# Optimization experiments

Measured on AMD Instinct MI355X. Metric: run time of the kernel, lower is better.

## Reference

```python
import jax, jax.numpy as jnp
import numpy as np

B, N, C, H = 8, 1024, 1024, 16
HD = C // H
SCALE = HD ** -0.5

def setup_inputs() -> dict:
    key = jax.random.key(0)
    k1, k2, k3, k4 = jax.random.split(key, 4)
    x = jax.random.normal(k1, (B, N, C), dtype=jnp.float32)
    # torch nn.Linear weights: [out, in]
    w_qkv = jax.random.normal(k2, (3 * C, C), dtype=jnp.float32) * (C ** -0.5)
    w_proj = jax.random.normal(k3, (C, C), dtype=jnp.float32) * (C ** -0.5)
    b_proj = jax.random.normal(k4, (C,), dtype=jnp.float32) * 0.02
    return {"x": x, "w_qkv": w_qkv, "w_proj": w_proj, "b_proj": b_proj}

def reference(x, w_qkv, w_proj, b_proj):
    Bv, Nv, Cv = x.shape
    # qkv projection (no bias); torch Linear: x @ W^T
    qkv = jnp.einsum('bnc,dc->bnd', x, w_qkv)
    qkv = qkv.reshape(Bv, Nv, 3, H, HD).transpose(2, 0, 3, 1, 4)  # [3,B,H,N,hd]
    q, k, v = qkv[0], qkv[1], qkv[2]
    attn = jnp.einsum('bhnd,bhmd->bhnm', q, k) * SCALE  # [B,H,N,N]
    attn = jax.nn.softmax(attn, axis=-1)
    out = jnp.einsum('bhnm,bhmd->bhnd', attn, v)
    out = out.transpose(0, 2, 1, 3).reshape(Bv, Nv, Cv)
    out = jnp.einsum('bnc,dc->bnd', out, w_proj) + b_proj
    return out
```

## Files before the change

kernel.cpp:

```cpp
#include <hip/hip_runtime.h>


typedef __attribute__((ext_vector_type(8))) short bf16x8;
typedef __attribute__((ext_vector_type(4))) short bf16x4;
typedef __attribute__((ext_vector_type(4))) float f32x4;

__device__ __forceinline__ short f2bf(float f) {
    union { float f; unsigned u; } x;
    x.f = f;
    unsigned r = x.u + 0x7fffu + ((x.u >> 16) & 1u);
    return (short)(r >> 16);
}

__device__ __forceinline__ void load_lds16(const void* g, void* l) {
    __builtin_amdgcn_global_load_lds((const __attribute__((address_space(1))) unsigned*)g,
                                     (__attribute__((address_space(3))) unsigned*)l,
                                     16, 0, 0);
}

__global__ __launch_bounds__(256) void convert_all(const float* __restrict__ x,
                                                   const float* __restrict__ wqkv,
                                                   const float* __restrict__ wproj,
                                                   short* __restrict__ xb,
                                                   short* __restrict__ wqkvb,
                                                   short* __restrict__ wprojb) {
    int i = blockIdx.x * 256 + threadIdx.x;
    const float* src;
    short* dst;
    int j;
    if (i < 2097152)      { src = x;     dst = xb;     j = i; }
    else if (i < 2883584) { src = wqkv;  dst = wqkvb;  j = i - 2097152; }
    else                  { src = wproj; dst = wprojb; j = i - 2883584; }
    float4 v = *(const float4*)(src + j * 4);
    unsigned lo = (unsigned short)f2bf(v.x) | ((unsigned)(unsigned short)f2bf(v.y) << 16);
    unsigned hi = (unsigned short)f2bf(v.z) | ((unsigned)(unsigned short)f2bf(v.w) << 16);
    uint2 p; p.x = lo; p.y = hi;
    *(uint2*)(dst + j * 4) = p;
}

__global__ __launch_bounds__(256, 4) void gemm_qkv(const short* __restrict__ A,
                                                   const short* __restrict__ Bt,
                                                   short* __restrict__ q,
                                                   short* __restrict__ k,
                                                   short* __restrict__ vt) {
    __shared__ alignas(16) short As[2][128][32];
    __shared__ alignas(16) short Bs[2][128][32];
    const int K = 1024;
    const int m0 = blockIdx.y * 128;
    const int n0 = blockIdx.x * 128;
    const int t = threadIdx.x;
    const int w = t >> 6, lane = t & 63, quad = lane >> 4, l16 = lane & 15;
    const int wm = (w >> 1) * 64, wn = (w & 1) * 64;
    const int srow = lane >> 2;
    const int sc8 = (((lane & 3) ^ ((lane >> 3) & 3))) * 8;
    const int cq  = (quad ^ ((l16 >> 1) & 3)) * 8;

    const short* Abase = &A[(m0 + w * 32 + srow) * K + sc8];
    const short* Bbase = &Bt[(n0 + w * 32 + srow) * K + sc8];

    f32x4 acc[4][4];
    for (int mi = 0; mi < 4; ++mi)
        for (int ni = 0; ni < 4; ++ni)
            acc[mi][ni] = (f32x4){0.f, 0.f, 0.f, 0.f};

    load_lds16(Abase,          &As[0][w * 32][0]);
    load_lds16(Abase + 16 * K, &As[0][w * 32 + 16][0]);
    load_lds16(Bbase,          &Bs[0][w * 32][0]);
    load_lds16(Bbase + 16 * K, &Bs[0][w * 32 + 16][0]);

    #pragma unroll
    for (int it = 0; it < 32; ++it) {
        const int cur = it & 1;
        asm volatile("s_waitcnt vmcnt(0) lgkmcnt(0)" ::: "memory");
        asm volatile("s_barrier" ::: "memory");
        if (it < 31) {
            const int nb = cur ^ 1;
            load_lds16(Abase + (it + 1) * 32,          &As[nb][w * 32][0]);
            load_lds16(Abase + 16 * K + (it + 1) * 32, &As[nb][w * 32 + 16][0]);
            load_lds16(Bbase + (it + 1) * 32,          &Bs[nb][w * 32][0]);
            load_lds16(Bbase + 16 * K + (it + 1) * 32, &Bs[nb][w * 32 + 16][0]);
        }
        bf16x8 af[4], bfr[4];
        for (int i = 0; i < 4; ++i) af[i]  = *(const bf16x8*)&As[cur][wm + i * 16 + l16][cq];
        for (int i = 0; i < 4; ++i) bfr[i] = *(const bf16x8*)&Bs[cur][wn + i * 16 + l16][cq];
        for (int mi = 0; mi < 4; ++mi)
            for (int ni = 0; ni < 4; ++ni)
                acc[mi][ni] = __builtin_amdgcn_mfma_f32_16x16x32_bf16(af[mi], bfr[ni], acc[mi][ni], 0, 0, 0);
    }

    const float QS = 0.125f * 1.44269504088896f;
    for (int ni = 0; ni < 4; ++ni) {
        int col = n0 + wn + ni * 16 + l16;
        int sect = col >> 10;
        int c = col & 1023;
        int h = c >> 6, d = c & 63;
        for (int mi = 0; mi < 4; ++mi) {
            for (int r = 0; r < 4; ++r) {
                int m = m0 + wm + mi * 16 + quad * 4 + r;
                int b = m >> 10, i = m & 1023;
                float v = acc[mi][ni][r];
                if (sect == 0)      q[((b * 16 + h) * 1024 + i) * 64 + d] = f2bf(v * QS);
                else if (sect == 1) k[((b * 16 + h) * 1024 + i) * 64 + d] = f2bf(v);
                else                vt[((b * 16 + h) * 64 + d) * 1024 + i] = f2bf(v);
            }
        }
    }
}

__global__ __launch_bounds__(256) void attn_kernel(const short* __restrict__ q,
                                                   const short* __restrict__ k,
                                                   const short* __restrict__ vt,
                                                   short* __restrict__ ao) {
    __shared__ alignas(16) short Ks[2][64][72];
    __shared__ alignas(16) short Vs[2][64][72];

    const int bh = blockIdx.y, qt = blockIdx.x;
    const int t = threadIdx.x, w = t >> 6, lane = t & 63, quad = lane >> 4, l16 = lane & 15;
    const short* qg = q  + (bh * 1024 + qt * 128) * 64;
    const short* kg = k  + bh * 65536;
    const short* vg = vt + bh * 65536;

    bf16x8 qf[2][2];
    for (int mi = 0; mi < 2; ++mi) {
        const short* qr = qg + (w * 32 + mi * 16 + l16) * 64;
        qf[mi][0] = *(const bf16x8*)(qr + quad * 8);
        qf[mi][1] = *(const bf16x8*)(qr + 32 + quad * 8);
    }

    const int r0 = t >> 3,          c80 = (t & 7) * 8;
    const int r1 = (t + 256) >> 3,  c81 = c80;

    float rs[2] = {0.f, 0.f};
    f32x4 oaccT[2][4];
    for (int mi = 0; mi < 2; ++mi)
        for (int dt = 0; dt < 4; ++dt) oaccT[mi][dt] = (f32x4){0.f, 0.f, 0.f, 0.f};

    {
        float4 a = *(const float4*)&kg[r0 * 64 + c80];
        float4 b = *(const float4*)&kg[r1 * 64 + c81];
        float4 c = *(const float4*)&vg[r0 * 1024 + c80];
        float4 d = *(const float4*)&vg[r1 * 1024 + c81];
        *(float4*)&Ks[0][r0][c80] = a;  *(float4*)&Ks[0][r1][c81] = b;
        *(float4*)&Vs[0][r0][c80] = c;  *(float4*)&Vs[0][r1][c81] = d;
    }

    for (int jt = 0; jt < 16; ++jt) {
        const int cur = jt & 1;
        asm volatile("s_waitcnt lgkmcnt(0)" ::: "memory");
        asm volatile("s_barrier" ::: "memory");

        float4 kr0, kr1, vr0, vr1;
        if (jt < 15) {
            int jn = jt + 1;
            kr0 = *(const float4*)&kg[(jn * 64 + r0) * 64 + c80];
            kr1 = *(const float4*)&kg[(jn * 64 + r1) * 64 + c81];
            vr0 = *(const float4*)&vg[r0 * 1024 + jn * 64 + c80];
            vr1 = *(const float4*)&vg[r1 * 1024 + jn * 64 + c81];
        }

        for (int js = 0; js < 4; ++js) {
            bf16x8 kf0 = *(const bf16x8*)&Ks[cur][js * 16 + l16][quad * 8];
            bf16x8 kf1 = *(const bf16x8*)&Ks[cur][js * 16 + l16][32 + quad * 8];
            bf16x4 vtf[4];
            for (int dt = 0; dt < 4; ++dt)
                vtf[dt] = *(const bf16x4*)&Vs[cur][dt * 16 + l16][js * 16 + quad * 4];
            for (int mi = 0; mi < 2; ++mi) {
                f32x4 s = (f32x4){0.f, 0.f, 0.f, 0.f};
                s = __builtin_amdgcn_mfma_f32_16x16x32_bf16(kf0, qf[mi][0], s, 0, 0, 0);
                s = __builtin_amdgcn_mfma_f32_16x16x32_bf16(kf1, qf[mi][1], s, 0, 0, 0);
                bf16x4 pfrag;
                for (int r = 0; r < 4; ++r) {
                    float p = __builtin_amdgcn_exp2f(s[r]);
                    rs[mi] += p;
                    pfrag[r] = f2bf(p);
                }
                for (int dt = 0; dt < 4; ++dt)
                    oaccT[mi][dt] = __builtin_amdgcn_mfma_f32_16x16x16bf16_1k(
                        vtf[dt], pfrag, oaccT[mi][dt], 0, 0, 0);
            }
        }

        if (jt < 15) {
            const int nxt = cur ^ 1;
            *(float4*)&Ks[nxt][r0][c80] = kr0;  *(float4*)&Ks[nxt][r1][c81] = kr1;
            *(float4*)&Vs[nxt][r0][c80] = vr0;  *(float4*)&Vs[nxt][r1][c81] = vr1;
        }
    }

    for (int mi = 0; mi < 2; ++mi) {
        rs[mi] += __shfl_xor(rs[mi], 16, 64);
        rs[mi] += __shfl_xor(rs[mi], 32, 64);
    }

    const int b = bh >> 4, h = bh & 15;
    for (int mi = 0; mi < 2; ++mi) {
        float inv = 1.0f / rs[mi];
        int i = qt * 128 + w * 32 + mi * 16 + l16;
        short* aor = ao + (b * 1024 + i) * 1024 + h * 64;
        for (int dt = 0; dt < 4; ++dt) {
            bf16x4 o4;
            for (int r = 0; r < 4; ++r) o4[r] = f2bf(oaccT[mi][dt][r] * inv);
            *(bf16x4*)(aor + dt * 16 + quad * 4) = o4;
        }
    }
}

__global__ __launch_bounds__(256, 4) void gemm_proj(const short* __restrict__ A,
                                                    const short* __restrict__ Bt,
                                                    const float* __restrict__ bias,
                                                    float* __restrict__ out) {
    __shared__ alignas(16) short As[2][128][32];
    __shared__ alignas(16) short Bs[2][128][32];
    const int K = 1024;
    const int m0 = blockIdx.y * 128;
    const int n0 = blockIdx.x * 128;
    const int t = threadIdx.x;
    const int w = t >> 6, lane = t & 63, quad = lane >> 4, l16 = lane & 15;
    const int wm = (w >> 1) * 64, wn = (w & 1) * 64;
    const int srow = lane >> 2;
    const int sc8 = (((lane & 3) ^ ((lane >> 3) & 3))) * 8;
    const int cq  = (quad ^ ((l16 >> 1) & 3)) * 8;

    const short* Abase = &A[(m0 + w * 32 + srow) * K + sc8];
    const short* Bbase = &Bt[(n0 + w * 32 + srow) * K + sc8];

    f32x4 acc[4][4];
    for (int mi = 0; mi < 4; ++mi)
        for (int ni = 0; ni < 4; ++ni)
            acc[mi][ni] = (f32x4){0.f, 0.f, 0.f, 0.f};

    load_lds16(Abase,          &As[0][w * 32][0]);
    load_lds16(Abase + 16 * K, &As[0][w * 32 + 16][0]);
    load_lds16(Bbase,          &Bs[0][w * 32][0]);
    load_lds16(Bbase + 16 * K, &Bs[0][w * 32 + 16][0]);

    #pragma unroll
    for (int it = 0; it < 32; ++it) {
        const int cur = it & 1;
        asm volatile("s_waitcnt vmcnt(0) lgkmcnt(0)" ::: "memory");
        asm volatile("s_barrier" ::: "memory");
        if (it < 31) {
            const int nb = cur ^ 1;
            load_lds16(Abase + (it + 1) * 32,          &As[nb][w * 32][0]);
            load_lds16(Abase + 16 * K + (it + 1) * 32, &As[nb][w * 32 + 16][0]);
            load_lds16(Bbase + (it + 1) * 32,          &Bs[nb][w * 32][0]);
            load_lds16(Bbase + 16 * K + (it + 1) * 32, &Bs[nb][w * 32 + 16][0]);
        }
        bf16x8 af[4], bfr[4];
        for (int i = 0; i < 4; ++i) af[i]  = *(const bf16x8*)&As[cur][wm + i * 16 + l16][cq];
        for (int i = 0; i < 4; ++i) bfr[i] = *(const bf16x8*)&Bs[cur][wn + i * 16 + l16][cq];
        for (int mi = 0; mi < 4; ++mi)
            for (int ni = 0; ni < 4; ++ni)
                acc[mi][ni] = __builtin_amdgcn_mfma_f32_16x16x32_bf16(af[mi], bfr[ni], acc[mi][ni], 0, 0, 0);
    }

    for (int ni = 0; ni < 4; ++ni) {
        int col = n0 + wn + ni * 16 + l16;
        float bv = bias[col];
        for (int mi = 0; mi < 4; ++mi) {
            for (int r = 0; r < 4; ++r) {
                int m = m0 + wm + mi * 16 + quad * 4 + r;
                out[m * 1024 + col] = acc[mi][ni][r] + bv;
            }
        }
    }
}

extern "C" void kernel_launch(void* const* d_in, const int* in_sizes, int n_in,
                              void* d_out, int out_size, void* d_ws, size_t ws_size,
                              hipStream_t stream) {
    const float* x      = (const float*)d_in[0];
    const float* w_qkv  = (const float*)d_in[1];
    const float* w_proj = (const float*)d_in[2];
    const float* b_proj = (const float*)d_in[3];
    float* out = (float*)d_out;

    char* ws = (char*)d_ws;
    short* xb     = (short*)(ws);
    short* wqkvb  = (short*)(ws + 16777216);
    short* wprojb = (short*)(ws + 23068672);
    short* qb     = (short*)(ws + 25165824);
    short* kb     = (short*)(ws + 41943040);
    short* vtb    = (short*)(ws + 58720256);
    short* aob    = (short*)(ws + 75497472);

    convert_all<<<12288, 256, 0, stream>>>(x, w_qkv, w_proj, xb, wqkvb, wprojb);
    gemm_qkv<<<dim3(24, 64), 256, 0, stream>>>(xb, wqkvb, qb, kb, vtb);
    attn_kernel<<<dim3(8, 128), 256, 0, stream>>>(qb, kb, vtb, aob);
    gemm_proj<<<dim3(8, 64), 256, 0, stream>>>(aob, wprojb, b_proj, out);
}
```

Baseline: 268.4 us.

## Replace both GEMMs with a 256x256 tile, 8-wave, deeply pipelined kernel

Both linear projections now use one templated GEMM with 256x256 output tiles, 512 threads, BK=64 and a double-buffered 128KB dynamic LDS layout with XOR swizzling. Global-to-LDS loads are spread across four MFMA phases with partial vmcnt waits, and s_setprio raises priority around the MFMA blocks. The aim is to raise arithmetic intensity and overlap loads with MFMA work. Block indices are remapped so neighbouring blocks share row panels in cache. The cost is fewer blocks, only 128 for the projection GEMM on 256 CUs, along with higher register and LDS pressure.

Result: no change. 266.9 us (-0.6%).

```diff
diff --git a/kernel.cpp b/kernel.cpp
--- a/kernel.cpp
+++ b/kernel.cpp
@@ -38,70 +38,175 @@
     *(uint2*)(dst + j * 4) = p;
 }
 
-__global__ __launch_bounds__(256, 4) void gemm_qkv(const short* __restrict__ A,
-                                                   const short* __restrict__ Bt,
-                                                   short* __restrict__ q,
-                                                   short* __restrict__ k,
-                                                   short* __restrict__ vt) {
-    __shared__ alignas(16) short As[2][128][32];
-    __shared__ alignas(16) short Bs[2][128][32];
+template<int EPI, int NTX>
+__global__ __launch_bounds__(512, 2) void gemm256(const short* __restrict__ A,
+                                                  const short* __restrict__ Bt,
+                                                  short* __restrict__ q,
+                                                  short* __restrict__ kk,
+                                                  short* __restrict__ vt,
+                                                  const float* __restrict__ bias,
+                                                  float* __restrict__ out) {
+    extern __shared__ short lds[];
+    short* const As = lds;
+    short* const Bs = lds + 32768;
     const int K = 1024;
-    const int m0 = blockIdx.y * 128;
-    const int n0 = blockIdx.x * 128;
+
+    constexpr int CHUNK = NTX * 4;
+    const int bid = blockIdx.x;
+    const int tile = (bid & 7) * CHUNK + (bid >> 3);
+    const int m0 = (tile / NTX) * 256;
+    const int n0 = (tile % NTX) * 256;
+
     const int t = threadIdx.x;
     const int w = t >> 6, lane = t & 63, quad = lane >> 4, l16 = lane & 15;
-    const int wm = (w >> 1) * 64, wn = (w & 1) * 64;
-    const int srow = lane >> 2;
-    const int sc8 = (((lane & 3) ^ ((lane >> 3) & 3))) * 8;
-    const int cq  = (quad ^ ((l16 >> 1) & 3)) * 8;
-
-    const short* Abase = &A[(m0 + w * 32 + srow) * K + sc8];
-    const short* Bbase = &Bt[(n0 + w * 32 + srow) * K + sc8];
-
-    f32x4 acc[4][4];
-    for (int mi = 0; mi < 4; ++mi)
-        for (int ni = 0; ni < 4; ++ni)
-            acc[mi][ni] = (f32x4){0.f, 0.f, 0.f, 0.f};
-
-    load_lds16(Abase,          &As[0][w * 32][0]);
-    load_lds16(Abase + 16 * K, &As[0][w * 32 + 16][0]);
-    load_lds16(Bbase,          &Bs[0][w * 32][0]);
-    load_lds16(Bbase + 16 * K, &Bs[0][w * 32 + 16][0]);
-
+    const int wm = (w >> 2) * 128, wn = (w & 3) * 64;
+    const int sw = l16 & 7;
+
+    const int srow = t >> 3;
+    const int scol = ((t & 7) ^ (srow & 7)) * 8;
+    const short* Ag = A  + (m0 + srow) * K + scol;
+    const short* Bg = Bt + (n0 + srow) * K + scol;
+    short* const Asw = As + (w * 8) * 64;
+    short* const Bsw = Bs + (w * 8) * 64;
+
+    f32x4 acc[8][4];
     #pragma unroll
-    for (int it = 0; it < 32; ++it) {
-        const int cur = it & 1;
-        asm volatile("s_waitcnt vmcnt(0) lgkmcnt(0)" ::: "memory");
-        asm volatile("s_barrier" ::: "memory");
-        if (it < 31) {
-            const int nb = cur ^ 1;
-            load_lds16(Abase + (it + 1) * 32,          &As[nb][w * 32][0]);
-            load_lds16(Abase + 16 * K + (it + 1) * 32, &As[nb][w * 32 + 16][0]);
-            load_lds16(Bbase + (it + 1) * 32,          &Bs[nb][w * 32][0]);
-            load_lds16(Bbase + 16 * K + (it + 1) * 32, &Bs[nb][w * 32 + 16][0]);
-        }
-        bf16x8 af[4], bfr[4];
-        for (int i = 0; i < 4; ++i) af[i]  = *(const bf16x8*)&As[cur][wm + i * 16 + l16][cq];
-        for (int i = 0; i < 4; ++i) bfr[i] = *(const bf16x8*)&Bs[cur][wn + i * 16 + l16][cq];
-        for (int mi = 0; mi < 4; ++mi)
-            for (int ni = 0; ni < 4; ++ni)
-                acc[mi][ni] = __builtin_amdgcn_mfma_f32_16x16x32_bf16(af[mi], bfr[ni], acc[mi][ni], 0, 0, 0);
-    }
-
-    const float QS = 0.125f * 1.44269504088896f;
-    for (int ni = 0; ni < 4; ++ni) {
-        int col = n0 + wn + ni * 16 + l16;
-        int sect = col >> 10;
-        int c = col & 1023;
-        int h = c >> 6, d = c & 63;
-        for (int mi = 0; mi < 4; ++mi) {
-            for (int r = 0; r < 4; ++r) {
-                int m = m0 + wm + mi * 16 + quad * 4 + r;
-                int b = m >> 10, i = m & 1023;
-                float v = acc[mi][ni][r];
-                if (sect == 0)      q[((b * 16 + h) * 1024 + i) * 64 + d] = f2bf(v * QS);
-                else if (sect == 1) k[((b * 16 + h) * 1024 + i) * 64 + d] = f2bf(v);
-                else                vt[((b * 16 + h) * 64 + d) * 1024 + i] = f2bf(v);
+    for (int mi = 0; mi < 8; ++mi)
+        #pragma unroll
+        for (int ni = 0; ni < 4; ++ni) acc[mi][ni] = (f32x4){0.f, 0.f, 0.f, 0.f};
+
+    bf16x8 af[4][2], bf[4][2];
+
+#define STG_A(kt_, d_, r_) load_lds16(Ag + (r_) * 64 * K + (kt_) * 64, Asw + (d_) * 16384 + (r_) * 4096)
+#define STG_B(kt_, d_, r_) load_lds16(Bg + (r_) * 64 * K + (kt_) * 64, Bsw + (d_) * 16384 + (r_) * 4096)
+
+    STG_A(0, 0, 0); STG_A(0, 0, 1); STG_A(0, 0, 2); STG_A(0, 0, 3);
+    STG_B(0, 0, 0); STG_B(0, 0, 1); STG_B(0, 0, 2); STG_B(0, 0, 3);
+    STG_A(1, 1, 0); STG_A(1, 1, 1); STG_A(1, 1, 2); STG_A(1, 1, 3);
+    STG_B(1, 1, 0); STG_B(1, 1, 1); STG_B(1, 1, 2); STG_B(1, 1, 3);
+    asm volatile("s_waitcnt vmcnt(8)" ::: "memory");
+    asm volatile("s_barrier" ::: "memory");
+
+    #pragma unroll
+    for (int kt = 0; kt < 16; ++kt) {
+        const int d = kt & 1;
+        const short* Ar = As + d * 16384;
+        const short* Br = Bs + d * 16384;
+
+        #pragma unroll
+        for (int mi = 0; mi < 4; ++mi)
+            #pragma unroll
+            for (int c = 0; c < 2; ++c)
+                af[mi][c] = *(const bf16x8*)(Ar + (wm + mi * 16 + l16) * 64 + (((quad + 4 * c) ^ sw) * 8));
+        #pragma unroll
+        for (int ni = 0; ni < 2; ++ni)
+            #pragma unroll
+            for (int c = 0; c < 2; ++c)
+                bf[ni][c] = *(const bf16x8*)(Br + (wn + ni * 16 + l16) * 64 + (((quad + 4 * c) ^ sw) * 8));
+        asm volatile("s_barrier" ::: "memory");
+        asm volatile("s_waitcnt lgkmcnt(0)" ::: "memory");
+        __builtin_amdgcn_sched_barrier(0);
+        __builtin_amdgcn_s_setprio(1);
+        #pragma unroll
+        for (int mi = 0; mi < 4; ++mi)
+            #pragma unroll
+            for (int ni = 0; ni < 2; ++ni) {
+                acc[mi][ni] = __builtin_amdgcn_mfma_f32_16x16x32_bf16(af[mi][0], bf[ni][0], acc[mi][ni], 0, 0, 0);
+                acc[mi][ni] = __builtin_amdgcn_mfma_f32_16x16x32_bf16(af[mi][1], bf[ni][1], acc[mi][ni], 0, 0, 0);
+            }
+        __builtin_amdgcn_s_setprio(0);
+        asm volatile("s_barrier" ::: "memory");
+
+        #pragma unroll
+        for (int ni = 2; ni < 4; ++ni)
+            #pragma unroll
+            for (int c = 0; c < 2; ++c)
+                bf[ni][c] = *(const bf16x8*)(Br + (wn + ni * 16 + l16) * 64 + (((quad + 4 * c) ^ sw) * 8));
+        if (kt < 14) { STG_A(kt + 2, d, 0); STG_A(kt + 2, d, 2); }
+        asm volatile("s_barrier" ::: "memory");
+        asm volatile("s_waitcnt lgkmcnt(0)" ::: "memory");
+        __builtin_amdgcn_sched_barrier(0);
+        __builtin_amdgcn_s_setprio(1);
+        #pragma unroll
+        for (int mi = 0; mi < 4; ++mi)
+            #pragma unroll
+            for (int ni = 2; ni < 4; ++ni) {
+                acc[mi][ni] = __builtin_amdgcn_mfma_f32_16x16x32_bf16(af[mi][0], bf[ni][0], acc[mi][ni], 0, 0, 0);
+                acc[mi][ni] = __builtin_amdgcn_mfma_f32_16x16x32_bf16(af[mi][1], bf[ni][1], acc[mi][ni], 0, 0, 0);
+            }
+        __builtin_amdgcn_s_setprio(0);
+        asm volatile("s_barrier" ::: "memory");
+
+        #pragma unroll
+        for (int mi = 0; mi < 4; ++mi)
+            #pragma unroll
+            for (int c = 0; c < 2; ++c)
+                af[mi][c] = *(const bf16x8*)(Ar + (wm + 64 + mi * 16 + l16) * 64 + (((quad + 4 * c) ^ sw) * 8));
+        if (kt < 14) { STG_B(kt + 2, d, 0); STG_B(kt + 2, d, 1); }
+        asm volatile("s_barrier" ::: "memory");
+        asm volatile("s_waitcnt lgkmcnt(0)" ::: "memory");
+        __builtin_amdgcn_sched_barrier(0);
+        __builtin_amdgcn_s_setprio(1);
+        #pragma unroll
+        for (int mi = 0; mi < 4; ++mi)
+            #pragma unroll
+            for (int ni = 0; ni < 2; ++ni) {
+                acc[mi + 4][ni] = __builtin_amdgcn_mfma_f32_16x16x32_bf16(af[mi][0], bf[ni][0], acc[mi + 4][ni], 0, 0, 0);
+                acc[mi + 4][ni] = __builtin_amdgcn_mfma_f32_16x16x32_bf16(af[mi][1], bf[ni][1], acc[mi + 4][ni], 0, 0, 0);
+            }
+        __builtin_amdgcn_s_setprio(0);
+        asm volatile("s_barrier" ::: "memory");
+
+        __builtin_amdgcn_s_setprio(1);
+        #pragma unroll
+        for (int mi = 0; mi < 4; ++mi)
+            #pragma unroll
+            for (int ni = 2; ni < 4; ++ni) {
+                acc[mi + 4][ni] = __builtin_amdgcn_mfma_f32_16x16x32_bf16(af[mi][0], bf[ni][0], acc[mi + 4][ni], 0, 0, 0);
+                acc[mi + 4][ni] = __builtin_amdgcn_mfma_f32_16x16x32_bf16(af[mi][1], bf[ni][1], acc[mi + 4][ni], 0, 0, 0);
+            }
+        __builtin_amdgcn_s_setprio(0);
+        if (kt < 14) { STG_B(kt + 2, d, 2); STG_B(kt + 2, d, 3); STG_A(kt + 2, d, 1); STG_A(kt + 2, d, 3); }
+        if (kt < 14)       asm volatile("s_waitcnt vmcnt(8)" ::: "memory");
+        else if (kt == 14) asm volatile("s_waitcnt vmcnt(0)" ::: "memory");
+        asm volatile("s_barrier" ::: "memory");
+    }
+#undef STG_A
+#undef STG_B
+
+    if (EPI == 0) {
+        const float QS = 0.125f * 1.44269504088896f;
+        #pragma unroll
+        for (int ni = 0; ni < 4; ++ni) {
+            int col = n0 + wn + ni * 16 + l16;
+            int sect = col >> 10;
+            int c = col & 1023;
+            int h = c >> 6, dd = c & 63;
+            #pragma unroll
+            for (int mi = 0; mi < 8; ++mi) {
+                #pragma unroll
+                for (int r = 0; r < 4; ++r) {
+                    int m = m0 + wm + mi * 16 + quad * 4 + r;
+                    int b = m >> 10, i = m & 1023;
+                    float v = acc[mi][ni][r];
+                    if (sect == 0)      q[((b * 16 + h) * 1024 + i) * 64 + dd] = f2bf(v * QS);
+                    else if (sect == 1) kk[((b * 16 + h) * 1024 + i) * 64 + dd] = f2bf(v);
+                    else                vt[((b * 16 + h) * 64 + dd) * 1024 + i] = f2bf(v);
+                }
+            }
+        }
+    } else {
+        #pragma unroll
+        for (int ni = 0; ni < 4; ++ni) {
+            int col = n0 + wn + ni * 16 + l16;
+            float bv = bias[col];
+            #pragma unroll
+            for (int mi = 0; mi < 8; ++mi) {
+                #pragma unroll
+                for (int r = 0; r < 4; ++r) {
+                    int m = m0 + wm + mi * 16 + quad * 4 + r;
+                    out[m * 1024 + col] = acc[mi][ni][r] + bv;
+                }
             }
         }
     }
@@ -205,67 +310,6 @@
     }
 }
 
-__global__ __launch_bounds__(256, 4) void gemm_proj(const short* __restrict__ A,
-                                                    const short* __restrict__ Bt,
-                                                    const float* __restrict__ bias,
-                                                    float* __restrict__ out) {
-    __shared__ alignas(16) short As[2][128][32];
-    __shared__ alignas(16) short Bs[2][128][32];
-    const int K = 1024;
-    const int m0 = blockIdx.y * 128;
-    const int n0 = blockIdx.x * 128;
-    const int t = threadIdx.x;
-    const int w = t >> 6, lane = t & 63, quad = lane >> 4, l16 = lane & 15;
-    const int wm = (w >> 1) * 64, wn = (w & 1) * 64;
-    const int srow = lane >> 2;
-    const int sc8 = (((lane & 3) ^ ((lane >> 3) & 3))) * 8;
-    const int cq  = (quad ^ ((l16 >> 1) & 3)) * 8;
-
-    const short* Abase = &A[(m0 + w * 32 + srow) * K + sc8];
-    const short* Bbase = &Bt[(n0 + w * 32 + srow) * K + sc8];
-
-    f32x4 acc[4][4];
-    for (int mi = 0; mi < 4; ++mi)
-        for (int ni = 0; ni < 4; ++ni)
-            acc[mi][ni] = (f32x4){0.f, 0.f, 0.f, 0.f};
-
-    load_lds16(Abase,          &As[0][w * 32][0]);
-    load_lds16(Abase + 16 * K, &As[0][w * 32 + 16][0]);
-    load_lds16(Bbase,          &Bs[0][w * 32][0]);
-    load_lds16(Bbase + 16 * K, &Bs[0][w * 32 + 16][0]);
-
-    #pragma unroll
-    for (int it = 0; it < 32; ++it) {
-        const int cur = it & 1;
-        asm volatile("s_waitcnt vmcnt(0) lgkmcnt(0)" ::: "memory");
-        asm volatile("s_barrier" ::: "memory");
-        if (it < 31) {
-            const int nb = cur ^ 1;
-            load_lds16(Abase + (it + 1) * 32,          &As[nb][w * 32][0]);
-            load_lds16(Abase + 16 * K + (it + 1) * 32, &As[nb][w * 32 + 16][0]);
-            load_lds16(Bbase + (it + 1) * 32,          &Bs[nb][w * 32][0]);
-            load_lds16(Bbase + 16 * K + (it + 1) * 32, &Bs[nb][w * 32 + 16][0]);
-        }
-        bf16x8 af[4], bfr[4];
-        for (int i = 0; i < 4; ++i) af[i]  = *(const bf16x8*)&As[cur][wm + i * 16 + l16][cq];
-        for (int i = 0; i < 4; ++i) bfr[i] = *(const bf16x8*)&Bs[cur][wn + i * 16 + l16][cq];
-        for (int mi = 0; mi < 4; ++mi)
-            for (int ni = 0; ni < 4; ++ni)
-                acc[mi][ni] = __builtin_amdgcn_mfma_f32_16x16x32_bf16(af[mi], bfr[ni], acc[mi][ni], 0, 0, 0);
-    }
-
-    for (int ni = 0; ni < 4; ++ni) {
-        int col = n0 + wn + ni * 16 + l16;
-        float bv = bias[col];
-        for (int mi = 0; mi < 4; ++mi) {
-            for (int r = 0; r < 4; ++r) {
-                int m = m0 + wm + mi * 16 + quad * 4 + r;
-                out[m * 1024 + col] = acc[mi][ni][r] + bv;
-            }
-        }
-    }
-}
-
 extern "C" void kernel_launch(void* const* d_in, const int* in_sizes, int n_in,
                               void* d_out, int out_size, void* d_ws, size_t ws_size,
                               hipStream_t stream) {
@@ -284,8 +328,17 @@
     short* vtb    = (short*)(ws + 58720256);
     short* aob    = (short*)(ws + 75497472);
 
+    static bool s_init = false;
+    if (!s_init) {
+        hipFuncSetAttribute(reinterpret_cast<const void*>(&gemm256<0, 12>),
+                            hipFuncAttributeMaxDynamicSharedMemorySize, 131072);
+        hipFuncSetAttribute(reinterpret_cast<const void*>(&gemm256<1, 4>),
+                            hipFuncAttributeMaxDynamicSharedMemorySize, 131072);
+        s_init = true;
+    }
+
     convert_all<<<12288, 256, 0, stream>>>(x, w_qkv, w_proj, xb, wqkvb, wprojb);
-    gemm_qkv<<<dim3(24, 64), 256, 0, stream>>>(xb, wqkvb, qb, kb, vtb);
+    gemm256<0, 12><<<384, 512, 131072, stream>>>(xb, wqkvb, qb, kb, vtb, nullptr, nullptr);
     attn_kernel<<<dim3(8, 128), 256, 0, stream>>>(qb, kb, vtb, aob);
-    gemm_proj<<<dim3(8, 64), 256, 0, stream>>>(aob, wprojb, b_proj, out);
-}
+    gemm256<1, 4><<<128, 512, 131072, stream>>>(aob, wprojb, nullptr, nullptr, nullptr, b_proj, out);
+}
```
